# Optimization experiments

Hardware: AMD Instinct MI355X
Metric: run time of the kernel (lower is better)

The kernel has to match this reference:

```python
import jax, jax.numpy as jnp
import numpy as np
from jax import lax

V, VE, DE, DX, HID, T, S = 100000, 1000, 256, 64, 512, 64, 2048
H = HID // 2


def setup_inputs() -> dict:
    key = jax.random.key(0)
    ks = jax.random.split(key, 18)
    def n(k, shape, scale=0.1):
        return jax.random.normal(k, shape, jnp.float32) * scale
    return {
        "sentence": jax.random.randint(ks[0], (S,), 0, V),
        "extra": jax.random.randint(ks[1], (S,), 0, VE),
        "b": 0,
        "e": S,
        "emb": n(ks[2], (V, DE)),
        "extra_emb": n(ks[3], (VE, DX)),
        "w_ih_f": n(ks[4], (4 * H, DE + DX)),
        "w_hh_f": n(ks[5], (4 * H, H)),
        "b_ih_f": n(ks[6], (4 * H,)),
        "b_hh_f": n(ks[7], (4 * H,)),
        "w_ih_b": n(ks[8], (4 * H, DE + DX)),
        "w_hh_b": n(ks[9], (4 * H, H)),
        "b_ih_b": n(ks[10], (4 * H,)),
        "b_hh_b": n(ks[11], (4 * H,)),
        "fc_w": n(ks[12], (T, HID)),
        "fc_b": n(ks[13], (T,)),
        "crf_start": n(ks[14], (T,)),
        "crf_end": n(ks[15], (T,)),
        "crf_trans": n(ks[16], (T, T)),
    }


def _lstm_dir(x, w_ih, w_hh, b_ih, b_hh):
    """Single-direction LSTM over x [S, D] with batch 1. PyTorch gate order i,f,g,o."""
    Hh = w_hh.shape[1]
    gx = x @ w_ih.T + (b_ih + b_hh)  # [S, 4H], input projection hoisted out of the scan

    def step(carry, g_in):
        h, c = carry
        g = g_in + h @ w_hh.T  # [4H]
        i, f, gg, o = jnp.split(g, 4)
        i = jax.nn.sigmoid(i)
        f = jax.nn.sigmoid(f)
        gg = jnp.tanh(gg)
        o = jax.nn.sigmoid(o)
        c = f * c + i * gg
        h = o * jnp.tanh(c)
        return (h, c), h

    init = (jnp.zeros((Hh,), x.dtype), jnp.zeros((Hh,), x.dtype))
    _, hs = lax.scan(step, init, gx)
    return hs  # [S, H]


def _lstm_feats(sentence, extra, emb, extra_emb,
                w_ih_f, w_hh_f, b_ih_f, b_hh_f,
                w_ih_b, w_hh_b, b_ih_b, b_hh_b, fc_w, fc_b):
    x = jnp.concatenate([emb[sentence], extra_emb[extra]], axis=1)  # [S, DE+DX]
    hf = _lstm_dir(x, w_ih_f, w_hh_f, b_ih_f, b_hh_f)              # [S, H]
    hb = _lstm_dir(x[::-1], w_ih_b, w_hh_b, b_ih_b, b_hh_b)[::-1]  # [S, H]
    lstm_out = jnp.concatenate([hf, hb], axis=1)                   # [S, 2H]
    return lstm_out @ fc_w.T + fc_b                                # [S, T]


def _viterbi_decode(feats, start, end, trans):
    """torchcrf-style Viterbi on feats [L, T]; returns best tag path [L] (int32)."""
    score0 = start + feats[0]  # [T]

    def step(score, emit_t):
        m = score[:, None] + trans + emit_t[None, :]  # [T_prev, T_next]
        return jnp.max(m, axis=0), jnp.argmax(m, axis=0).astype(jnp.int32)

    final_score, bps = lax.scan(step, score0, feats[1:])  # bps: [L-1, T]
    final_score = final_score + end
    last_tag = jnp.argmax(final_score).astype(jnp.int32)

    def back(tag, bp_t):
        prev = bp_t[tag]
        return prev, prev

    _, prev_tags = lax.scan(back, last_tag, bps[::-1])
    return jnp.concatenate([prev_tags[::-1], last_tag[None]])  # [L]


def reference(sentence, extra, b, e, emb, extra_emb,
              w_ih_f, w_hh_f, b_ih_f, b_hh_f,
              w_ih_b, w_hh_b, b_ih_b, b_hh_b,
              fc_w, fc_b, crf_start, crf_end, crf_trans):
    feats = _lstm_feats(sentence, extra, emb, extra_emb,
                        w_ih_f, w_hh_f, b_ih_f, b_hh_f,
                        w_ih_b, w_hh_b, b_ih_b, b_hh_b, fc_w, fc_b)
    feats = feats[b:e]  # static Python-int phrase bounds
    return _viterbi_decode(feats, crf_start, crf_end, crf_trans)
```

## Files before the change

kernel.cpp:

```cpp
#include <hip/hip_runtime.h>
#include <stdint.h>

#define SEQ   2048
#define DE    256
#define DXX   64
#define DIN   320
#define HH    256
#define G4    1024
#define NT    64

static constexpr size_t OFF_GX = 0;
static constexpr size_t OFF_H  = OFF_GX + (size_t)2 * SEQ * G4;
static constexpr size_t HSTR   = (size_t)SEQ * HH;
static constexpr size_t OFF_SL = OFF_H + 2 * HSTR;
static constexpr size_t OFF_FE = OFF_SL + 2048;
static constexpr size_t OFF_BP = OFF_FE + (size_t)SEQ * NT;
static constexpr size_t WS_NEEDED_BYTES = OFF_BP * 4 + (size_t)SEQ * NT;

__global__ __launch_bounds__(256) void k_init(unsigned long long* __restrict__ slot) {
  const int tid = threadIdx.x;
  #pragma unroll
  for (int b = 0; b < 4; ++b) slot[b * 256 + tid] = 0ull;
}

__global__ __launch_bounds__(512) void k_gx(
    const int* __restrict__ sent, const int* __restrict__ extra,
    const float* __restrict__ emb, const float* __restrict__ xemb,
    const float* __restrict__ wf, const float* __restrict__ wb,
    const float* __restrict__ bif, const float* __restrict__ bhf,
    const float* __restrict__ bib, const float* __restrict__ bhb,
    float* __restrict__ GX) {
  __shared__ __align__(16) float xs[32][36];
  __shared__ __align__(16) float wl[32][260];
  const int tid = threadIdx.x;
  const int s0 = blockIdx.x * 32, r0 = blockIdx.y * 256, dir = blockIdx.z;
  const float* W = dir ? wb : wf;
  const int tids = tid & 7;
  const int tidr = tid >> 3;
  float acc[4][4];
  #pragma unroll
  for (int a = 0; a < 4; ++a)
    #pragma unroll
    for (int b = 0; b < 4; ++b) acc[a][b] = 0.f;

  for (int kc = 0; kc < 10; ++kc) {
    const int k0 = kc * 32;
    __syncthreads();
    for (int e = tid; e < 1024; e += 512) {
      int kk = e & 31, sl = e >> 5;
      int s = s0 + sl;
      int src = dir ? (SEQ - 1 - s) : s;
      int k = k0 + kk;
      float v;
      if (k < DE) v = emb[(size_t)sent[src] * DE + k];
      else        v = xemb[(size_t)extra[src] * DXX + (k - DE)];
      xs[kk][sl] = v;
    }
    for (int e = tid; e < 8192; e += 512) {
      int kk = e & 31, rl = e >> 5;
      wl[kk][rl] = W[(size_t)(r0 + rl) * DIN + k0 + kk];
    }
    __syncthreads();
    #pragma unroll
    for (int kk = 0; kk < 32; ++kk) {
      float4 xv = *(const float4*)&xs[kk][4 * tids];
      float4 wv = *(const float4*)&wl[kk][4 * tidr];
      acc[0][0] += xv.x * wv.x; acc[0][1] += xv.x * wv.y; acc[0][2] += xv.x * wv.z; acc[0][3] += xv.x * wv.w;
      acc[1][0] += xv.y * wv.x; acc[1][1] += xv.y * wv.y; acc[1][2] += xv.y * wv.z; acc[1][3] += xv.y * wv.w;
      acc[2][0] += xv.z * wv.x; acc[2][1] += xv.z * wv.y; acc[2][2] += xv.z * wv.z; acc[2][3] += xv.z * wv.w;
      acc[3][0] += xv.w * wv.x; acc[3][1] += xv.w * wv.y; acc[3][2] += xv.w * wv.z; acc[3][3] += xv.w * wv.w;
    }
  }
  const float* BI = dir ? bib : bif;
  const float* BH = dir ? bhb : bhf;
  float4 b1 = *(const float4*)&BI[r0 + 4 * tidr];
  float4 b2 = *(const float4*)&BH[r0 + 4 * tidr];
  float bx = b1.x + b2.x, by = b1.y + b2.y, bz = b1.z + b2.z, bw = b1.w + b2.w;
  #pragma unroll
  for (int ss = 0; ss < 4; ++ss) {
    int s = s0 + 4 * tids + ss;
    float4 o;
    o.x = acc[ss][0] + bx; o.y = acc[ss][1] + by; o.z = acc[ss][2] + bz; o.w = acc[ss][3] + bw;
    *(float4*)&GX[((size_t)dir * SEQ + s) * G4 + r0 + 4 * tidr] = o;
  }
}

__global__ __launch_bounds__(256, 1) void k_lstm16(
    const float* __restrict__ whf, const float* __restrict__ whb,
    const float* __restrict__ GX, float* __restrict__ H,
    unsigned long long* __restrict__ slot) {
  const int dir = blockIdx.x >> 4;
  const int p   = blockIdx.x & 15;
  const int tid = threadIdx.x;
  const int rr  = tid >> 2;
  const int q   = tid & 3;
  const int gq  = rr >> 4;
  const int joq = rr & 15;
  const int rowQ = (gq << 8) | (p << 4) | joq;
  const int rowC = ((tid >> 4) << 8) | (p << 4) | (tid & 15);

  const float4* w4g =
      (const float4*)((dir ? whb : whf) + (size_t)rowQ * HH) + q * 16;
  float4 w[16];
  #pragma unroll
  for (int i = 0; i < 16; ++i) w[i] = w4g[i];
  #pragma unroll
  for (int i = 0; i < 16; ++i)
    asm volatile("" : "+v"(w[i].x), "+v"(w[i].y), "+v"(w[i].z), "+v"(w[i].w));

  const float* gxc = GX + (size_t)dir * SEQ * G4 + rowC;
  float* Hd = H + (size_t)dir * HSTR;
  unsigned long long* sl = slot + dir * 512;

  __shared__ __align__(16) float hl[4][68];
  __shared__ float psum[256];
  __shared__ float gacc[64];
  float c = 0.f;
  int budget = 1 << 18;

  for (int t = 0; t < SEQ; ++t) {
    float gxv = 0.f;
    if (tid < 64) gxv = gxc[(size_t)t * G4];
    {
      unsigned long long* sp = &sl[(t & 1) * 256 + tid];
      unsigned long long v;
      do {
        v = __hip_atomic_load(sp, __ATOMIC_RELAXED, __HIP_MEMORY_SCOPE_AGENT);
      } while ((unsigned)(v >> 32) != (unsigned)t && --budget > 0);
      union { unsigned u; float f; } cv; cv.u = (unsigned)v;
      hl[tid >> 6][tid & 63] = cv.f;
    }
    __syncthreads();
    const float4* h4 = (const float4*)(hl[q]);
    float a0 = 0.f, a1 = 0.f, a2 = 0.f, a3 = 0.f;
    #pragma unroll
    for (int i = 0; i < 16; ++i) {
      float4 wv = w[i];
      float4 hv = h4[i];
      a0 += wv.x * hv.x; a1 += wv.y * hv.y; a2 += wv.z * hv.z; a3 += wv.w * hv.w;
    }
    psum[tid] = (a0 + a1) + (a2 + a3);
    __syncthreads();
    if (tid < 64) {
      float s = gxv + ((psum[4 * tid] + psum[4 * tid + 1]) +
                       (psum[4 * tid + 2] + psum[4 * tid + 3]));
      gacc[tid] = s;
    }
    if (tid < 16) {
      float iv = gacc[tid], fv = gacc[16 + tid], gv = gacc[32 + tid],
            ov = gacc[48 + tid];
      float ig = 1.f / (1.f + expf(-iv));
      float fg = 1.f / (1.f + expf(-fv));
      float gg = tanhf(gv);
      float og = 1.f / (1.f + expf(-ov));
      c = fg * c + ig * gg;
      float h = og * tanhf(c);
      int jj = (p << 4) | tid;
      union { float f; unsigned u; } hu; hu.f = h;
      unsigned long long pk =
          ((unsigned long long)(unsigned)(t + 1) << 32) | hu.u;
      __hip_atomic_store(&sl[((t + 1) & 1) * 256 + jj], pk, __ATOMIC_RELAXED,
                         __HIP_MEMORY_SCOPE_AGENT);
      Hd[(size_t)t * HH + jj] = h;
    }
  }
}

__global__ __launch_bounds__(256) void k_feats(
    const float* __restrict__ HF, const float* __restrict__ HB,
    const float* __restrict__ fcw, const float* __restrict__ fcb,
    float* __restrict__ FE) {
  __shared__ float hlds[16][512];
  __shared__ float wl[64][65];
  const int tid = threadIdx.x;
  const int s0 = blockIdx.x * 16;
  for (int e = tid; e < 16 * 512; e += 256) {
    int sl = e >> 9, k = e & 511;
    float v = (k < HH) ? HF[(size_t)(s0 + sl) * HH + k]
                       : HB[(size_t)(SEQ - 1 - (s0 + sl)) * HH + (k - HH)];
    hlds[sl][k] = v;
  }
  const int j = tid & 63, sg = tid >> 6;
  float acc[4];
  #pragma unroll
  for (int q = 0; q < 4; ++q) acc[q] = fcb[j];
  for (int kc = 0; kc < 8; ++kc) {
    __syncthreads();
    for (int e = tid; e < 4096; e += 256) {
      int kk = e & 63, jj = e >> 6;
      wl[kk][jj] = fcw[(size_t)jj * 512 + kc * 64 + kk];
    }
    __syncthreads();
    #pragma unroll 8
    for (int kk = 0; kk < 64; ++kk) {
      float wv = wl[kk][j];
      int kg = kc * 64 + kk;
      #pragma unroll
      for (int q = 0; q < 4; ++q) acc[q] += hlds[4 * sg + q][kg] * wv;
    }
  }
  #pragma unroll
  for (int q = 0; q < 4; ++q)
    FE[(size_t)(s0 + 4 * sg + q) * NT + j] = acc[q];
}

__global__ __launch_bounds__(256) void k_viterbi(
    const float* __restrict__ feats, const float* __restrict__ start,
    const float* __restrict__ endv, const float* __restrict__ trans,
    unsigned char* __restrict__ bp, int* __restrict__ out) {
  __shared__ float tr[64 * 64];
  __shared__ float sc[64];
  __shared__ float pval[4][64];
  __shared__ int pidx[4][64];
  const int tid = threadIdx.x;
  for (int e = tid; e < 4096; e += 256) tr[e] = trans[e];
  if (tid < 64) sc[tid] = start[tid] + feats[tid];
  __syncthreads();
  const int w = tid >> 6, j = tid & 63;
  for (int t = 1; t < SEQ; ++t) {
    float fj = feats[t * NT + j];
    float best = -3.0e38f; int bi = 0;
    const int ibase = w << 4;
    #pragma unroll
    for (int ii = 0; ii < 16; ++ii) {
      int i = ibase + ii;
      float v = (sc[i] + tr[(i << 6) | j]) + fj;
      if (v > best) { best = v; bi = i; }
    }
    pval[w][j] = best; pidx[w][j] = bi;
    __syncthreads();
    if (w == 0) {
      float b = pval[0][j]; int x = pidx[0][j];
      if (pval[1][j] > b) { b = pval[1][j]; x = pidx[1][j]; }
      if (pval[2][j] > b) { b = pval[2][j]; x = pidx[2][j]; }
      if (pval[3][j] > b) { b = pval[3][j]; x = pidx[3][j]; }
      bp[t * NT + j] = (unsigned char)x;
      sc[j] = b;
    }
    __syncthreads();
  }
  if (tid == 0) {
    float best = -3.0e38f; int bt = 0;
    for (int i = 0; i < 64; ++i) {
      float v = sc[i] + endv[i];
      if (v > best) { best = v; bt = i; }
    }
    out[SEQ - 1] = bt;
    int tag = bt;
    for (int t = SEQ - 1; t >= 1; --t) {
      tag = bp[t * NT + tag];
      out[t - 1] = tag;
    }
  }
}

extern "C" void kernel_launch(void* const* d_in, const int* in_sizes, int n_in,
                              void* d_out, int out_size, void* d_ws, size_t ws_size,
                              hipStream_t stream) {
  if (n_in < 19) return;
  if (in_sizes[0] != SEQ || in_sizes[1] != SEQ) return;
  if (in_sizes[2] != 1 || in_sizes[3] != 1) return;
  if (in_sizes[4] != 100000 * DE) return;
  if (in_sizes[5] != 1000 * DXX) return;
  if (in_sizes[6] != G4 * DIN || in_sizes[7] != G4 * HH) return;
  if (in_sizes[8] != G4 || in_sizes[9] != G4) return;
  if (in_sizes[10] != G4 * DIN || in_sizes[11] != G4 * HH) return;
  if (in_sizes[14] != NT * 512 || in_sizes[15] != NT) return;
  if (in_sizes[16] != NT || in_sizes[17] != NT) return;
  if (in_sizes[18] != NT * NT) return;
  if (out_size < SEQ) return;
  if (ws_size < WS_NEEDED_BYTES) return;

  const int*   sent = (const int*)d_in[0];
  const int*   extra = (const int*)d_in[1];
  const float* emb  = (const float*)d_in[4];
  const float* xemb = (const float*)d_in[5];
  const float* wihf = (const float*)d_in[6];
  const float* whhf = (const float*)d_in[7];
  const float* bihf = (const float*)d_in[8];
  const float* bhhf = (const float*)d_in[9];
  const float* wihb = (const float*)d_in[10];
  const float* whhb = (const float*)d_in[11];
  const float* bihb = (const float*)d_in[12];
  const float* bhhb = (const float*)d_in[13];
  const float* fcw  = (const float*)d_in[14];
  const float* fcb  = (const float*)d_in[15];
  const float* cst  = (const float*)d_in[16];
  const float* cen  = (const float*)d_in[17];
  const float* ctr  = (const float*)d_in[18];

  float* ws = (float*)d_ws;
  float* GX = ws + OFF_GX;
  float* H  = ws + OFF_H;
  unsigned long long* SLOT = (unsigned long long*)(ws + OFF_SL);
  float* FE = ws + OFF_FE;
  unsigned char* BP = (unsigned char*)(ws + OFF_BP);

  k_init<<<1, 256, 0, stream>>>(SLOT);
  k_gx<<<dim3(SEQ / 32, G4 / 256, 2), 512, 0, stream>>>(
      sent, extra, emb, xemb, wihf, wihb, bihf, bhhf, bihb, bhhb, GX);
  k_lstm16<<<32, 256, 0, stream>>>(whhf, whhb, GX, H, SLOT);
  k_feats<<<SEQ / 16, 256, 0, stream>>>(H, H + HSTR, fcw, fcb, FE);
  k_viterbi<<<1, 256, 0, stream>>>(FE, cst, cen, ctr, BP, (int*)d_out);
}
```

Measured before the change: 5.055 ms.

## Skip polling own hidden slice, pipeline spin loads, compute gates via shuffles

Each block now writes its own 16 hidden values straight into LDS and skips polling them through global atomics. Other slices are polled with four outstanding atomic loads in rotation to cut the latency of the spin loop. Gate activations are computed in parallel across 64 lanes and combined with wavefront shuffles, replacing the gacc LDS round trip and the serial 16-lane activation step. Together these aim to shorten the per-timestep critical path of the sequential LSTM recurrence. The risk is extra memory traffic from the additional in-flight polls.

```diff
diff --git a/kernel.cpp b/kernel.cpp
--- a/kernel.cpp
+++ b/kernel.cpp
@@ -114,19 +114,34 @@
 
   __shared__ __align__(16) float hl[4][68];
   __shared__ float psum[256];
-  __shared__ float gacc[64];
   float c = 0.f;
   int budget = 1 << 18;
+  const bool ownpoll = ((tid >> 4) == p);
+
+  if (ownpoll) hl[tid >> 6][tid & 63] = 0.f;
 
   for (int t = 0; t < SEQ; ++t) {
     float gxv = 0.f;
     if (tid < 64) gxv = gxc[(size_t)t * G4];
-    {
+    if (!ownpoll) {
       unsigned long long* sp = &sl[(t & 1) * 256 + tid];
+      const unsigned tw = (unsigned)t;
       unsigned long long v;
-      do {
-        v = __hip_atomic_load(sp, __ATOMIC_RELAXED, __HIP_MEMORY_SCOPE_AGENT);
-      } while ((unsigned)(v >> 32) != (unsigned)t && --budget > 0);
+      unsigned long long v0 = __hip_atomic_load(sp, __ATOMIC_RELAXED, __HIP_MEMORY_SCOPE_AGENT);
+      unsigned long long v1 = __hip_atomic_load(sp, __ATOMIC_RELAXED, __HIP_MEMORY_SCOPE_AGENT);
+      unsigned long long v2 = __hip_atomic_load(sp, __ATOMIC_RELAXED, __HIP_MEMORY_SCOPE_AGENT);
+      unsigned long long v3 = __hip_atomic_load(sp, __ATOMIC_RELAXED, __HIP_MEMORY_SCOPE_AGENT);
+      for (;;) {
+        if ((unsigned)(v0 >> 32) == tw) { v = v0; break; }
+        v0 = __hip_atomic_load(sp, __ATOMIC_RELAXED, __HIP_MEMORY_SCOPE_AGENT);
+        if ((unsigned)(v1 >> 32) == tw) { v = v1; break; }
+        v1 = __hip_atomic_load(sp, __ATOMIC_RELAXED, __HIP_MEMORY_SCOPE_AGENT);
+        if ((unsigned)(v2 >> 32) == tw) { v = v2; break; }
+        v2 = __hip_atomic_load(sp, __ATOMIC_RELAXED, __HIP_MEMORY_SCOPE_AGENT);
+        if ((unsigned)(v3 >> 32) == tw) { v = v3; break; }
+        v3 = __hip_atomic_load(sp, __ATOMIC_RELAXED, __HIP_MEMORY_SCOPE_AGENT);
+        if (--budget <= 0) { v = v3; break; }
+      }
       union { unsigned u; float f; } cv; cv.u = (unsigned)v;
       hl[tid >> 6][tid & 63] = cv.f;
     }
@@ -144,24 +159,26 @@
     if (tid < 64) {
       float s = gxv + ((psum[4 * tid] + psum[4 * tid + 1]) +
                        (psum[4 * tid + 2] + psum[4 * tid + 3]));
-      gacc[tid] = s;
-    }
-    if (tid < 16) {
-      float iv = gacc[tid], fv = gacc[16 + tid], gv = gacc[32 + tid],
-            ov = gacc[48 + tid];
-      float ig = 1.f / (1.f + expf(-iv));
-      float fg = 1.f / (1.f + expf(-fv));
-      float gg = tanhf(gv);
-      float og = 1.f / (1.f + expf(-ov));
-      c = fg * c + ig * gg;
-      float h = og * tanhf(c);
-      int jj = (p << 4) | tid;
-      union { float f; unsigned u; } hu; hu.f = h;
-      unsigned long long pk =
-          ((unsigned long long)(unsigned)(t + 1) << 32) | hu.u;
-      __hip_atomic_store(&sl[((t + 1) & 1) * 256 + jj], pk, __ATOMIC_RELAXED,
-                         __HIP_MEMORY_SCOPE_AGENT);
-      Hd[(size_t)t * HH + jj] = h;
+      const int gg_ = tid >> 4;
+      const int ee  = tid & 15;
+      float sig = 1.f / (1.f + expf(-s));
+      float th  = tanhf(s);
+      float gated = (gg_ == 2) ? th : sig;
+      float fg = __shfl(gated, 16 + ee);
+      float gv = __shfl(gated, 32 + ee);
+      float og = __shfl(gated, 48 + ee);
+      if (tid < 16) {
+        c = fg * c + gated * gv;
+        float h = og * tanhf(c);
+        int jj = (p << 4) | tid;
+        union { float f; unsigned u; } hu; hu.f = h;
+        unsigned long long pk =
+            ((unsigned long long)(unsigned)(t + 1) << 32) | hu.u;
+        __hip_atomic_store(&sl[((t + 1) & 1) * 256 + jj], pk, __ATOMIC_RELAXED,
+                           __HIP_MEMORY_SCOPE_AGENT);
+        hl[jj >> 6][jj & 63] = h;
+        Hd[(size_t)t * HH + jj] = h;
+      }
     }
   }
 }
```

After: 4.984 ms. About the same (-1.4%).

## Run Viterbi in a single wavefront using shuffles and register-held transitions

Applied to the files above, without the earlier changes.

The Viterbi forward pass now runs as one 64-lane wavefront. Each lane keeps its transition column in registers and broadcasts the previous scores with __shfl. This removes the two block-wide __syncthreads per timestep and the cross-wave max reduction through shared memory. The next step's emission is also prefetched. In exchange, each step runs 64 serial compares per lane instead of 16, and the kernel uses more registers.

```diff
diff --git a/kernel.cpp b/kernel.cpp
--- a/kernel.cpp
+++ b/kernel.cpp
@@ -204,47 +204,36 @@
     FE[(size_t)(s0 + 4 * sg + q) * NT + j] = acc[q];
 }
 
-__global__ __launch_bounds__(256) void k_viterbi(
+__global__ __launch_bounds__(64) void k_viterbi(
     const float* __restrict__ feats, const float* __restrict__ start,
     const float* __restrict__ endv, const float* __restrict__ trans,
     unsigned char* __restrict__ bp, int* __restrict__ out) {
-  __shared__ float tr[64 * 64];
-  __shared__ float sc[64];
-  __shared__ float pval[4][64];
-  __shared__ int pidx[4][64];
-  const int tid = threadIdx.x;
-  for (int e = tid; e < 4096; e += 256) tr[e] = trans[e];
-  if (tid < 64) sc[tid] = start[tid] + feats[tid];
-  __syncthreads();
-  const int w = tid >> 6, j = tid & 63;
+  const int j = threadIdx.x;
+  float trc[64];
+  #pragma unroll
+  for (int i = 0; i < 64; ++i) trc[i] = trans[(i << 6) | j];
+  float sc = start[j] + feats[j];
+  float fj_next = feats[NT + j];
   for (int t = 1; t < SEQ; ++t) {
-    float fj = feats[t * NT + j];
+    float fj = fj_next;
+    if (t + 1 < SEQ) fj_next = feats[(t + 1) * NT + j];
     float best = -3.0e38f; int bi = 0;
-    const int ibase = w << 4;
-    #pragma unroll
-    for (int ii = 0; ii < 16; ++ii) {
-      int i = ibase + ii;
-      float v = (sc[i] + tr[(i << 6) | j]) + fj;
+    #pragma unroll
+    for (int i = 0; i < 64; ++i) {
+      float v = (__shfl(sc, i) + trc[i]) + fj;
       if (v > best) { best = v; bi = i; }
     }
-    pval[w][j] = best; pidx[w][j] = bi;
-    __syncthreads();
-    if (w == 0) {
-      float b = pval[0][j]; int x = pidx[0][j];
-      if (pval[1][j] > b) { b = pval[1][j]; x = pidx[1][j]; }
-      if (pval[2][j] > b) { b = pval[2][j]; x = pidx[2][j]; }
-      if (pval[3][j] > b) { b = pval[3][j]; x = pidx[3][j]; }
-      bp[t * NT + j] = (unsigned char)x;
-      sc[j] = b;
-    }
-    __syncthreads();
-  }
-  if (tid == 0) {
-    float best = -3.0e38f; int bt = 0;
-    for (int i = 0; i < 64; ++i) {
-      float v = sc[i] + endv[i];
-      if (v > best) { best = v; bt = i; }
-    }
+    bp[t * NT + j] = (unsigned char)bi;
+    sc = best;
+  }
+  float fin = sc + endv[j];
+  float best = -3.0e38f; int bt = 0;
+  #pragma unroll
+  for (int i = 0; i < 64; ++i) {
+    float v = __shfl(fin, i);
+    if (v > best) { best = v; bt = i; }
+  }
+  if (j == 0) {
     out[SEQ - 1] = bt;
     int tag = bt;
     for (int t = SEQ - 1; t >= 1; --t) {
@@ -301,5 +290,5 @@
       sent, extra, emb, xemb, wihf, wihb, bihf, bhhf, bihb, bhhb, GX);
   k_lstm16<<<32, 256, 0, stream>>>(whhf, whhb, GX, H, SLOT);
   k_feats<<<SEQ / 16, 256, 0, stream>>>(H, H + HSTR, fcw, fcb, FE);
-  k_viterbi<<<1, 256, 0, stream>>>(FE, cst, cen, ctr, BP, (int*)d_out);
-}
+  k_viterbi<<<1, 64, 0, stream>>>(FE, cst, cen, ctr, BP, (int*)d_out);
+}
```

Result: slower. 8.855 ms (+75.2%).
